# Kernel tuning notes

Measured on AMD Instinct MI355X. Metric: run time of the kernel, lower is better.

Reference implementation:

```python
import jax, jax.numpy as jnp
import numpy as np

N = 100_000   # nodes
E = 1_600_000 # edges
G = 128       # graphs in batch
DIN, DOUT = 100, 200


def setup_inputs() -> dict:
    key = jax.random.key(0)
    ks = jax.random.split(key, 12)
    def lin_w(k, fan_in, fan_out):
        return (jax.random.normal(k, (fan_in, fan_out), jnp.float32) / np.sqrt(fan_in)).astype(jnp.float32)
    return {
        "x": jax.random.normal(ks[0], (N, DIN), jnp.float32),
        "edge_index": jax.random.randint(ks[1], (2, E), 0, N, dtype=jnp.int32),
        "batch": jnp.sort(jax.random.randint(ks[2], (N,), 0, G, dtype=jnp.int32)),
        "W1": lin_w(ks[3], DIN, DOUT),  "b1": jnp.zeros((DOUT,), jnp.float32),
        "Wc": lin_w(ks[4], DOUT, DOUT), "bc": jnp.zeros((DOUT,), jnp.float32),
        "W2": lin_w(ks[5], DOUT, DOUT), "b2": jnp.zeros((DOUT,), jnp.float32),
        "W3": lin_w(ks[6], DOUT, DOUT), "b3": jnp.zeros((DOUT,), jnp.float32),
        "Wcls": lin_w(ks[7], DOUT, 2),  "bcls": jnp.zeros((2,), jnp.float32),
    }


def gcn_conv(x, W, b, src, dst, n_nodes):
    """PyG GCNConv: D^{-1/2}(A+I)D^{-1/2} X W + b, symmetric norm with self-loops."""
    h = x @ W  # [N, Dout]
    # degree at targets including the self-loop (+1)
    deg = jax.ops.segment_sum(jnp.ones((src.shape[0],), x.dtype), dst, num_segments=n_nodes) + 1.0
    dinv = jax.lax.rsqrt(deg)  # [N]
    # gather -> normalize -> scatter-add (messages along edges)
    msg = h[src] * (dinv[src] * dinv[dst])[:, None]          # [E, Dout]
    agg = jax.ops.segment_sum(msg, dst, num_segments=n_nodes)  # [N, Dout]
    # self-loop contribution handled analytically: norm_ii = dinv[i]^2
    agg = agg + h * (dinv * dinv)[:, None]
    return agg + b


def reference(x, edge_index, batch, W1, b1, Wc, bc, W2, b2, W3, b3, Wcls, bcls):
    src, dst = edge_index[0], edge_index[1]
    h = jax.nn.relu(gcn_conv(x, W1, b1, src, dst, N))
    # dropout is identity at eval time
    h = h @ Wc + bc
    h = jax.nn.relu(gcn_conv(h, W2, b2, src, dst, N))
    h = gcn_conv(h, W3, b3, src, dst, N)
    pooled = jax.ops.segment_max(h, batch, num_segments=G)  # global max pool -> [G, Dout]
    logits = pooled @ Wcls + bcls
    return jax.nn.softmax(logits, axis=1)
```

## Files before the change

### kernel.cpp

```cpp
#include <hip/hip_runtime.h>
#include <stdint.h>

#define N_NODES 100000
#define N_EDGES 1600000
#define N_GRAPHS 128
#define DIN 100
#define DOUT 200
#define LDH 200
#define LDX 128

#define NB 391
#define BCAP 5120
#define EPB 2048
#define NBLK 782

typedef unsigned short u16;
typedef unsigned int u32;
typedef _Float16 f16;
typedef f16 half8 __attribute__((ext_vector_type(8)));
typedef f16 half4 __attribute__((ext_vector_type(4)));
typedef f16 half2v __attribute__((ext_vector_type(2)));
typedef float floatx4 __attribute__((ext_vector_type(4)));

__device__ __forceinline__ float h2f(u16 h) {
  f16 x; __builtin_memcpy(&x, &h, 2); return (float)x;
}
__device__ __forceinline__ u16 f2h(float f) {
  f16 x = (f16)f; u16 r; __builtin_memcpy(&r, &x, 2); return r;
}
__device__ __forceinline__ u32 encmax(float f) {
  u32 b; __builtin_memcpy(&b, &f, 4);
  return (b & 0x80000000u) ? ~b : (b | 0x80000000u);
}

__device__ __forceinline__ void pack_frag(const float* __restrict__ W, int K, int nfrag,
                                          u16* __restrict__ out, int idx) {
  if (idx >= nfrag) return;
  int lane = idx & 63;
  int t = idx >> 6;
  int ct = t % 13, ks = t / 13;
  int n = ct * 16 + (lane & 15);
  int kbase = ks * 32 + (lane >> 4) * 8;
  u16 v[8];
  #pragma unroll
  for (int j = 0; j < 8; ++j) {
    int k = kbase + j;
    float f = (k < K && n < DOUT) ? W[(size_t)k * DOUT + n] : 0.f;
    v[j] = f2h(f);
  }
  uint4 o;
  o.x = (u32)v[0] | ((u32)v[1] << 16);
  o.y = (u32)v[2] | ((u32)v[3] << 16);
  o.z = (u32)v[4] | ((u32)v[5] << 16);
  o.w = (u32)v[6] | ((u32)v[7] << 16);
  *(uint4*)(out + (size_t)idx * 8) = o;
}

#define B_COMB  158
#define B_PK1   171
#define B_PK3   194
#define B_TOT   (194 + NBLK)
__global__ void k_prep(const int* __restrict__ dst, int* __restrict__ histAll,
                       const float* __restrict__ Wc, const float* __restrict__ bc,
                       const float* __restrict__ W2, float* __restrict__ Wc2,
                       float* __restrict__ bc2, const float* __restrict__ W1,
                       const float* __restrict__ W3, u16* __restrict__ Wpk1,
                       u16* __restrict__ Wpk3) {
  int b = blockIdx.x, t = threadIdx.x;
  if (b < B_COMB) {
    int gid = b * 256 + t;
    if (gid >= 201 * DOUT) return;
    int r = gid / DOUT, c = gid % DOUT;
    const float* a = (r < DOUT) ? (Wc + (size_t)r * DOUT) : bc;
    float s = 0.f;
    for (int k = 0; k < DOUT; ++k) s += a[k] * W2[(size_t)k * DOUT + c];
    if (r < DOUT) Wc2[(size_t)r * DOUT + c] = s;
    else bc2[c] = s;
  } else if (b < B_PK1) {
    pack_frag(W1, DIN, 4 * 13 * 64, Wpk1, (b - B_COMB) * 256 + t);
  } else if (b < B_PK3) {
    pack_frag(W3, DOUT, 7 * 13 * 64, Wpk3, (b - B_PK1) * 256 + t);
  } else {
    __shared__ int hist[NB];
    int hb = b - B_PK3;
    int e0 = hb * EPB;
    int e1 = min(e0 + EPB, N_EDGES);
    for (int j = t; j < NB; j += 256) hist[j] = 0;
    __syncthreads();
    for (int i = e0 + t; i < e1; i += 256)
      atomicAdd(&hist[dst[i] >> 8], 1);
    __syncthreads();
    for (int j = t; j < NB; j += 256)
      histAll[(size_t)hb * NB + j] = hist[j];
  }
}

#define SCAN_TOT (NB + 23)
__global__ void k_scan(const int* __restrict__ histAll, int* __restrict__ baseAll,
                       int* __restrict__ gcur, const float* __restrict__ Wc2,
                       u16* __restrict__ Wpk2) {
  int j = blockIdx.x, t = threadIdx.x;
  if (j >= NB) {
    pack_frag(Wc2, DOUT, 7 * 13 * 64, Wpk2, (j - NB) * 256 + t);
    return;
  }
  __shared__ int s[256];
  int run = 0;
  for (int c = 0; c < NBLK; c += 256) {
    int idx = c + t;
    int v = (idx < NBLK) ? histAll[(size_t)idx * NB + j] : 0;
    s[t] = v;
    __syncthreads();
    for (int o = 1; o < 256; o <<= 1) {
      int x = (t >= o) ? s[t - o] : 0;
      __syncthreads();
      s[t] += x;
      __syncthreads();
    }
    if (idx < NBLK) baseAll[(size_t)idx * NB + j] = run + s[t] - v;
    run += s[255];
    __syncthreads();
  }
  if (t == 0) gcur[j] = run;
}

__global__ void k_scatter(const int* __restrict__ src, const int* __restrict__ dst,
                          const int* __restrict__ baseAll, uint2* __restrict__ ebuf) {
  __shared__ int cur[NB];
  int b = blockIdx.x, t = threadIdx.x;
  int e0 = b * EPB;
  int e1 = min(e0 + EPB, N_EDGES);
  for (int j = t; j < NB; j += 256) cur[j] = baseAll[(size_t)b * NB + j];
  __syncthreads();
  for (int i = e0 + t; i < e1; i += 256) {
    int d = dst[i];
    int bk = d >> 8;
    int pos = atomicAdd(&cur[bk], 1);
    if (pos < BCAP)
      ebuf[(size_t)bk * BCAP + pos] = make_uint2((u32)d, (u32)src[i]);
  }
}

__global__ void k_csr(const uint2* __restrict__ ebuf, const int* __restrict__ gcur,
                      int* __restrict__ rowptr, float* __restrict__ dinv,
                      int* __restrict__ colv, const float* __restrict__ x,
                      u16* __restrict__ xs, u32* __restrict__ partenc) {
  __shared__ int s_cnt[256];
  __shared__ int s_cur[256];
  __shared__ int s_scan[256];
  __shared__ int s_g[NB];
  __shared__ int s_red[256];
  __shared__ float s_dinv[256];
  int b = blockIdx.x, t = threadIdx.x;
  int zid = b * 256 + t;
  if (zid < N_GRAPHS * DOUT) partenc[zid] = 0u;
  for (int j = t; j < NB; j += 256) s_g[j] = gcur[j];
  s_cnt[t] = 0;
  __syncthreads();
  int pacc = 0;
  for (int i = t; i < b; i += 256) pacc += s_g[i];
  s_red[t] = pacc;
  __syncthreads();
  for (int o = 128; o > 0; o >>= 1) {
    if (t < o) s_red[t] += s_red[t + o];
    __syncthreads();
  }
  int base = s_red[0];
  if (b == NB - 1 && t == 0) rowptr[N_NODES] = base + s_g[b];
  int cnt = s_g[b];
  int node0 = b << 8;
  const uint2* eb = ebuf + (size_t)b * BCAP;
  for (int i = t; i < cnt; i += 256)
    atomicAdd(&s_cnt[eb[i].x & 255], 1);
  __syncthreads();
  int v = s_cnt[t];
  s_scan[t] = v;
  __syncthreads();
  for (int o = 1; o < 256; o <<= 1) {
    int x2 = (t >= o) ? s_scan[t - o] : 0;
    __syncthreads();
    s_scan[t] += x2;
    __syncthreads();
  }
  int run = s_scan[t] - v;
  s_cur[t] = base + run;
  float dval = rsqrtf((float)v + 1.0f);
  s_dinv[t] = dval;
  int node = node0 + t;
  if (node < N_NODES) {
    rowptr[node] = base + run;
    dinv[node] = dval;
  }
  __syncthreads();
  for (int i = t; i < cnt; i += 256) {
    uint2 e = eb[i];
    int pos = atomicAdd(&s_cur[e.x & 255], 1);
    colv[pos] = (int)e.y;
  }
  for (int idx = t; idx < 256 * 50; idx += 256) {
    int nl = idx / 50, c = idx % 50;
    int nd = node0 + nl;
    if (nd < N_NODES) {
      float d = s_dinv[nl];
      float2 vv = *(const float2*)(x + (size_t)nd * DIN + c * 2);
      half2v o; o[0] = (f16)(d * vv.x); o[1] = (f16)(d * vv.y);
      *(half2v*)(xs + (size_t)nd * LDX + c * 2) = o;
    }
  }
}

template <int NKS>
__global__ __launch_bounds__(256) void k_gemm_mfma(const u16* __restrict__ A, int lda,
                                                   const u16* __restrict__ Wpk,
                                                   const float* __restrict__ bias,
                                                   const float* __restrict__ rowscale,
                                                   u16* __restrict__ C, int relu, int nrows) {
  int wv = threadIdx.x >> 6;
  int lane = threadIdx.x & 63;
  int r0 = blockIdx.x * 128 + wv * 32;
  int m = lane & 15, q = lane >> 4;
  int row0 = r0 + m, row1 = r0 + 16 + m;
  bool ok0 = (row0 < nrows), ok1 = (row1 < nrows);
  const u16* a0p = A + (size_t)row0 * lda + q * 8;
  const u16* a1p = A + (size_t)row1 * lda + q * 8;

  floatx4 acc0[13], acc1[13];
  #pragma unroll
  for (int ct = 0; ct < 13; ++ct) {
    acc0[ct] = floatx4{0.f, 0.f, 0.f, 0.f};
    acc1[ct] = floatx4{0.f, 0.f, 0.f, 0.f};
  }

  const u16* wp = Wpk + (size_t)lane * 8;
  #pragma unroll
  for (int ks = 0; ks < NKS; ++ks) {
    half8 a0 = ok0 ? *(const half8*)(a0p + ks * 32) : half8{0, 0, 0, 0, 0, 0, 0, 0};
    half8 a1 = ok1 ? *(const half8*)(a1p + ks * 32) : half8{0, 0, 0, 0, 0, 0, 0, 0};
    #pragma unroll
    for (int ct = 0; ct < 13; ++ct) {
      half8 bfr = *(const half8*)(wp + (size_t)(ks * 13 + ct) * 512);
      acc0[ct] = __builtin_amdgcn_mfma_f32_16x16x32_f16(a0, bfr, acc0[ct], 0, 0, 0);
      acc1[ct] = __builtin_amdgcn_mfma_f32_16x16x32_f16(a1, bfr, acc1[ct], 0, 0, 0);
    }
  }

  float sc0[4], sc1[4];
  #pragma unroll
  for (int rg = 0; rg < 4; ++rg) {
    int or0 = r0 + q * 4 + rg;
    int or1 = r0 + 16 + q * 4 + rg;
    sc0[rg] = (rowscale && or0 < nrows) ? rowscale[or0] : 1.f;
    sc1[rg] = (rowscale && or1 < nrows) ? rowscale[or1] : 1.f;
  }

  #pragma unroll
  for (int ct = 0; ct < 13; ++ct) {
    int c = ct * 16 + m;
    if (c >= DOUT) continue;
    float bv = bias ? bias[c] : 0.f;
    #pragma unroll
    for (int rg = 0; rg < 4; ++rg) {
      int or0 = r0 + q * 4 + rg;
      if (or0 < nrows) {
        float v = acc0[ct][rg] + bv;
        if (relu) v = fmaxf(v, 0.f);
        C[(size_t)or0 * LDH + c] = f2h(v * sc0[rg]);
      }
      int or1 = r0 + 16 + q * 4 + rg;
      if (or1 < nrows) {
        float v = acc1[ct][rg] + bv;
        if (relu) v = fmaxf(v, 0.f);
        C[(size_t)or1 * LDH + c] = f2h(v * sc1[rg]);
      }
    }
  }
}

__global__ void k_agg200h(const u16* __restrict__ T, const float* __restrict__ dinv,
                          const int* __restrict__ rowptr, const int* __restrict__ col,
                          const float* __restrict__ bias, u16* __restrict__ OUT,
                          int relu) {
  int wave = (blockIdx.x * blockDim.x + threadIdx.x) >> 6;
  int lane = threadIdx.x & 63;
  if (wave >= N_NODES || lane >= 50) return;
  int node = wave;
  int c4 = lane * 4;
  int beg = __builtin_amdgcn_readfirstlane(rowptr[node]);
  int end = __builtin_amdgcn_readfirstlane(rowptr[node + 1]);
  half4 sv = *(const half4*)(T + (size_t)node * LDH + c4);
  float di = dinv[node];
  float ax = 0.f, ay = 0.f, az = 0.f, aw = 0.f;
  int e = beg;
  for (; e + 16 <= end; e += 16) {
    int s[16];
    half4 tv[16];
    #pragma unroll
    for (int j = 0; j < 16; ++j) s[j] = col[e + j];
    #pragma unroll
    for (int j = 0; j < 16; ++j)
      tv[j] = *(const half4*)(T + (size_t)s[j] * LDH + c4);
    #pragma unroll
    for (int j = 0; j < 16; ++j) {
      ax += (float)tv[j][0]; ay += (float)tv[j][1];
      az += (float)tv[j][2]; aw += (float)tv[j][3];
    }
  }
  if (e + 8 <= end) {
    int s[8];
    half4 tv[8];
    #pragma unroll
    for (int j = 0; j < 8; ++j) s[j] = col[e + j];
    #pragma unroll
    for (int j = 0; j < 8; ++j)
      tv[j] = *(const half4*)(T + (size_t)s[j] * LDH + c4);
    #pragma unroll
    for (int j = 0; j < 8; ++j) {
      ax += (float)tv[j][0]; ay += (float)tv[j][1];
      az += (float)tv[j][2]; aw += (float)tv[j][3];
    }
    e += 8;
  }
  if (e + 4 <= end) {
    int s[4];
    half4 tv[4];
    #pragma unroll
    for (int j = 0; j < 4; ++j) s[j] = col[e + j];
    #pragma unroll
    for (int j = 0; j < 4; ++j)
      tv[j] = *(const half4*)(T + (size_t)s[j] * LDH + c4);
    #pragma unroll
    for (int j = 0; j < 4; ++j) {
      ax += (float)tv[j][0]; ay += (float)tv[j][1];
      az += (float)tv[j][2]; aw += (float)tv[j][3];
    }
    e += 4;
  }
  for (; e < end; ++e) {
    half4 tv = *(const half4*)(T + (size_t)col[e] * LDH + c4);
    ax += (float)tv[0]; ay += (float)tv[1];
    az += (float)tv[2]; aw += (float)tv[3];
  }
  float rx = di * (ax + (float)sv[0]);
  float ry = di * (ay + (float)sv[1]);
  float rz = di * (az + (float)sv[2]);
  float rw = di * (aw + (float)sv[3]);
  if (bias) {
    rx += bias[c4 + 0]; ry += bias[c4 + 1];
    rz += bias[c4 + 2]; rw += bias[c4 + 3];
  }
  if (relu) {
    rx = fmaxf(rx, 0.f); ry = fmaxf(ry, 0.f);
    rz = fmaxf(rz, 0.f); rw = fmaxf(rw, 0.f);
  }
  half4 o;
  o[0] = (f16)rx; o[1] = (f16)ry; o[2] = (f16)rz; o[3] = (f16)rw;
  __builtin_nontemporal_store(o, (half4*)(OUT + (size_t)node * LDH + c4));
}

__global__ void k_agg100h(const u16* __restrict__ T, const float* __restrict__ dinv,
                          const int* __restrict__ rowptr, const int* __restrict__ col,
                          u16* __restrict__ OUT) {
  int wave = (blockIdx.x * blockDim.x + threadIdx.x) >> 6;
  int lane = threadIdx.x & 63;
  if (wave >= N_NODES || lane >= 50) return;
  int node = wave;
  int c2 = lane * 2;
  int beg = __builtin_amdgcn_readfirstlane(rowptr[node]);
  int end = __builtin_amdgcn_readfirstlane(rowptr[node + 1]);
  half2v sv = *(const half2v*)(T + (size_t)node * LDX + c2);
  float di = dinv[node];
  float ax = 0.f, ay = 0.f;
  int e = beg;
  for (; e + 16 <= end; e += 16) {
    int s[16];
    half2v tv[16];
    #pragma unroll
    for (int j = 0; j < 16; ++j) s[j] = col[e + j];
    #pragma unroll
    for (int j = 0; j < 16; ++j)
      tv[j] = *(const half2v*)(T + (size_t)s[j] * LDX + c2);
    #pragma unroll
    for (int j = 0; j < 16; ++j) { ax += (float)tv[j][0]; ay += (float)tv[j][1]; }
  }
  if (e + 8 <= end) {
    int s[8];
    half2v tv[8];
    #pragma unroll
    for (int j = 0; j < 8; ++j) s[j] = col[e + j];
    #pragma unroll
    for (int j = 0; j < 8; ++j)
      tv[j] = *(const half2v*)(T + (size_t)s[j] * LDX + c2);
    #pragma unroll
    for (int j = 0; j < 8; ++j) { ax += (float)tv[j][0]; ay += (float)tv[j][1]; }
    e += 8;
  }
  if (e + 4 <= end) {
    int s[4];
    half2v tv[4];
    #pragma unroll
    for (int j = 0; j < 4; ++j) s[j] = col[e + j];
    #pragma unroll
    for (int j = 0; j < 4; ++j)
      tv[j] = *(const half2v*)(T + (size_t)s[j] * LDX + c2);
    #pragma unroll
    for (int j = 0; j < 4; ++j) { ax += (float)tv[j][0]; ay += (float)tv[j][1]; }
    e += 4;
  }
  for (; e < end; ++e) {
    half2v tv = *(const half2v*)(T + (size_t)col[e] * LDX + c2);
    ax += (float)tv[0]; ay += (float)tv[1];
  }
  half2v o;
  o[0] = (f16)(di * (ax + (float)sv[0]));
  o[1] = (f16)(di * (ay + (float)sv[1]));
  __builtin_nontemporal_store(o, (half2v*)(OUT + (size_t)node * LDX + c2));
}

__global__ void k_aggpool(const u16* __restrict__ T, const float* __restrict__ dinv,
                          const int* __restrict__ rowptr, const int* __restrict__ col,
                          const float* __restrict__ bias, const int* __restrict__ batch,
                          u32* __restrict__ partenc) {
  __shared__ u32 s_enc[4][DOUT];
  int t = threadIdx.x;
  for (int i = t; i < 4 * DOUT; i += 256) ((u32*)s_enc)[i] = 0u;
  __syncthreads();
  int wv = t >> 6, lane = t & 63;
  int nb0 = blockIdx.x * 16;
  int n0 = nb0 + wv * 4;
  int gfirst = batch[nb0];
  int rpl = rowptr[n0 + (lane < 4 ? lane : 4)];
  if (lane < 50) {
    int c4 = lane * 4;
    float b0 = bias[c4 + 0], b1v = bias[c4 + 1], b2v = bias[c4 + 2], b3v = bias[c4 + 3];
    for (int i = 0; i < 4; ++i) {
      int node = n0 + i;
      int beg = __builtin_amdgcn_readlane(rpl, i);
      int end = __builtin_amdgcn_readlane(rpl, i + 1);
      half4 sv = *(const half4*)(T + (size_t)node * LDH + c4);
      float di = dinv[node];
      float ax = 0.f, ay = 0.f, az = 0.f, aw = 0.f;
      int e = beg;
      for (; e + 16 <= end; e += 16) {
        int s[16];
        half4 tv[16];
        #pragma unroll
        for (int j = 0; j < 16; ++j) s[j] = col[e + j];
        #pragma unroll
        for (int j = 0; j < 16; ++j)
          tv[j] = *(const half4*)(T + (size_t)s[j] * LDH + c4);
        #pragma unroll
        for (int j = 0; j < 16; ++j) {
          ax += (float)tv[j][0]; ay += (float)tv[j][1];
          az += (float)tv[j][2]; aw += (float)tv[j][3];
        }
      }
      if (e + 8 <= end) {
        int s[8];
        half4 tv[8];
        #pragma unroll
        for (int j = 0; j < 8; ++j) s[j] = col[e + j];
        #pragma unroll
        for (int j = 0; j < 8; ++j)
          tv[j] = *(const half4*)(T + (size_t)s[j] * LDH + c4);
        #pragma unroll
        for (int j = 0; j < 8; ++j) {
          ax += (float)tv[j][0]; ay += (float)tv[j][1];
          az += (float)tv[j][2]; aw += (float)tv[j][3];
        }
        e += 8;
      }
      if (e + 4 <= end) {
        int s[4];
        half4 tv[4];
        #pragma unroll
        for (int j = 0; j < 4; ++j) s[j] = col[e + j];
        #pragma unroll
        for (int j = 0; j < 4; ++j)
          tv[j] = *(const half4*)(T + (size_t)s[j] * LDH + c4);
        #pragma unroll
        for (int j = 0; j < 4; ++j) {
          ax += (float)tv[j][0]; ay += (float)tv[j][1];
          az += (float)tv[j][2]; aw += (float)tv[j][3];
        }
        e += 4;
      }
      for (; e < end; ++e) {
        half4 tv = *(const half4*)(T + (size_t)col[e] * LDH + c4);
        ax += (float)tv[0]; ay += (float)tv[1];
        az += (float)tv[2]; aw += (float)tv[3];
      }
      float rx = di * (ax + (float)sv[0]) + b0;
      float ry = di * (ay + (float)sv[1]) + b1v;
      float rz = di * (az + (float)sv[2]) + b2v;
      float rw = di * (aw + (float)sv[3]) + b3v;
      u32 e0 = encmax(rx), e1 = encmax(ry), e2 = encmax(rz), e3 = encmax(rw);
      int slot = batch[node] - gfirst;
      if (slot < 4) {
        atomicMax(&s_enc[slot][c4 + 0], e0);
        atomicMax(&s_enc[slot][c4 + 1], e1);
        atomicMax(&s_enc[slot][c4 + 2], e2);
        atomicMax(&s_enc[slot][c4 + 3], e3);
      } else {
        u32* p = partenc + (size_t)batch[node] * DOUT + c4;
        atomicMax(&p[0], e0); atomicMax(&p[1], e1);
        atomicMax(&p[2], e2); atomicMax(&p[3], e3);
      }
    }
  }
  __syncthreads();
  for (int i = t; i < 4 * DOUT; i += 256) {
    u32 v = ((u32*)s_enc)[i];
    if (v) {
      int slot = i / DOUT, d = i % DOUT;
      atomicMax(&partenc[(size_t)(gfirst + slot) * DOUT + d], v);
    }
  }
}

__global__ void k_poolcls(const u32* __restrict__ partenc, const float* __restrict__ Wcls,
                          const float* __restrict__ bcls, float* __restrict__ out) {
  __shared__ float l0s[256], l1s[256];
  int g = blockIdx.x, t = threadIdx.x;
  float c0 = 0.f, c1 = 0.f;
  if (t < DOUT) {
    u32 e = partenc[(size_t)g * DOUT + t];
    float mv;
    if (e == 0u) {
      mv = -3.4e38f;
    } else {
      u32 b = (e & 0x80000000u) ? (e ^ 0x80000000u) : ~e;
      __builtin_memcpy(&mv, &b, 4);
    }
    c0 = mv * Wcls[t * 2 + 0];
    c1 = mv * Wcls[t * 2 + 1];
  }
  l0s[t] = c0; l1s[t] = c1;
  __syncthreads();
  for (int o = 128; o > 0; o >>= 1) {
    if (t < o) { l0s[t] += l0s[t + o]; l1s[t] += l1s[t + o]; }
    __syncthreads();
  }
  if (t == 0) {
    float l0 = l0s[0] + bcls[0], l1 = l1s[0] + bcls[1];
    float m = fmaxf(l0, l1);
    float e0 = expf(l0 - m), e1 = expf(l1 - m);
    float inv = 1.0f / (e0 + e1);
    out[g * 2 + 0] = e0 * inv;
    out[g * 2 + 1] = e1 * inv;
  }
}

static inline size_t align256(size_t x) { return (x + 255) & ~(size_t)255; }

extern "C" void kernel_launch(void* const* d_in, const int* in_sizes, int n_in,
                              void* d_out, int out_size, void* d_ws, size_t ws_size,
                              hipStream_t stream) {
  const float* x     = (const float*)d_in[0];
  const int*   ei    = (const int*)d_in[1];
  const int*   batch = (const int*)d_in[2];
  const float* W1    = (const float*)d_in[3];
  const float* b1    = (const float*)d_in[4];
  const float* Wc    = (const float*)d_in[5];
  const float* bc    = (const float*)d_in[6];
  const float* W2    = (const float*)d_in[7];
  const float* b2    = (const float*)d_in[8];
  const float* W3    = (const float*)d_in[9];
  const float* b3    = (const float*)d_in[10];
  const float* Wcls  = (const float*)d_in[11];
  const float* bcls  = (const float*)d_in[12];
  float* out = (float*)d_out;

  const int N = N_NODES, E = N_EDGES;
  const int* src = ei;
  const int* dst = ei + E;

  char* ws = (char*)d_ws;
  size_t off = 0;
  float* dinv    = (float*)(ws + off); off = align256(off + (size_t)N * 4);
  int*   rowptr  = (int*)  (ws + off); off = align256(off + (size_t)(N + 1) * 4);
  int*   col     = (int*)  (ws + off); off = align256(off + (size_t)E * 4);
  int*   gcur    = (int*)  (ws + off); off = align256(off + (size_t)NB * 4);
  int*   histAll = (int*)  (ws + off); off = align256(off + (size_t)NBLK * NB * 4);
  int*   baseAll = (int*)  (ws + off); off = align256(off + (size_t)NBLK * NB * 4);
  float* Wc2     = (float*)(ws + off); off = align256(off + (size_t)DOUT * DOUT * 4);
  float* bc2     = (float*)(ws + off); off = align256(off + (size_t)DOUT * 4);
  u16*   Wpk1    = (u16*)  (ws + off); off = align256(off + (size_t)4 * 13 * 64 * 8 * 2);
  u16*   Wpk2    = (u16*)  (ws + off); off = align256(off + (size_t)7 * 13 * 64 * 8 * 2);
  u16*   Wpk3    = (u16*)  (ws + off); off = align256(off + (size_t)7 * 13 * 64 * 8 * 2);
  u16*   xs      = (u16*)  (ws + off); off = align256(off + ((size_t)N * LDX + 128) * 2);
  u16*   bufX    = (u16*)  (ws + off); off = align256(off + ((size_t)N * LDX + 128) * 2);
  u16*   buf0    = (u16*)  (ws + off); off = align256(off + ((size_t)N * LDH + 128) * 2);
  u16*   buf1    = (u16*)  (ws + off); off = align256(off + ((size_t)N * LDH + 128) * 2);
  u16*   buf2    = (u16*)  (ws + off); off = align256(off + ((size_t)N * LDH + 128) * 2);

  uint2* ebuf    = (uint2*)buf0;
  u32*   partenc = (u32*)histAll;

  k_prep<<<B_TOT, 256, 0, stream>>>(dst, histAll, Wc, bc, W2, Wc2, bc2,
                                    W1, W3, Wpk1, Wpk3);
  k_scan<<<SCAN_TOT, 256, 0, stream>>>(histAll, baseAll, gcur, Wc2, Wpk2);
  k_scatter<<<NBLK, 256, 0, stream>>>(src, dst, baseAll, ebuf);
  k_csr<<<NB, 256, 0, stream>>>(ebuf, gcur, rowptr, dinv, col, x, xs, partenc);

  int gemmb = (N + 127) / 128;
  int aggb  = (N + 3) / 4;
  int aggpb = N / 16;

  k_agg100h<<<aggb, 256, 0, stream>>>(xs, dinv, rowptr, col, bufX);
  k_gemm_mfma<4><<<gemmb, 256, 0, stream>>>(bufX, LDX, Wpk1, b1, nullptr, buf0, 1, N);
  k_gemm_mfma<7><<<gemmb, 256, 0, stream>>>(buf0, LDH, Wpk2, bc2, dinv, buf2, 0, N);
  k_agg200h<<<aggb, 256, 0, stream>>>(buf2, dinv, rowptr, col, b2, buf0, 1);
  k_gemm_mfma<7><<<gemmb, 256, 0, stream>>>(buf0, LDH, Wpk3, nullptr, dinv, buf1, 0, N);
  k_aggpool<<<aggpb, 256, 0, stream>>>(buf1, dinv, rowptr, col, b3, batch, partenc);
  k_poolcls<<<N_GRAPHS, 256, 0, stream>>>(partenc, Wcls, bcls, out);
}
```

Before: 647.3 us.

## Fuse first-layer aggregation into MFMA GEMM and pack edge buffer to u32

The first GCN layer's neighbor aggregation and its GEMM are fused into one kernel. Each wave aggregates 32 rows into an LDS tile and then runs the MFMA product from it, so the intermediate aggregated buffer is no longer written to and read back from global memory. The scatter stage now packs source index and local destination into a single u32 instead of a uint2, halving edge-bucket traffic. The pooling kernel keeps a running max per graph segment and issues atomics only when the segment changes. The fused kernel has far fewer waves in flight during the latency-bound gather, since each wave handles 32 nodes in sequence, which may reduce latency hiding.

Measured after the change: 672.2 us. +3.9%, slower.

```diff
diff --git a/kernel.cpp b/kernel.cpp
--- a/kernel.cpp
+++ b/kernel.cpp
@@ -8,6 +8,7 @@
 #define DOUT 200
 #define LDH 200
 #define LDX 128
+#define LDT 136
 
 #define NB 391
 #define BCAP 5120
@@ -125,7 +126,7 @@
 }
 
 __global__ void k_scatter(const int* __restrict__ src, const int* __restrict__ dst,
-                          const int* __restrict__ baseAll, uint2* __restrict__ ebuf) {
+                          const int* __restrict__ baseAll, u32* __restrict__ ebuf) {
   __shared__ int cur[NB];
   int b = blockIdx.x, t = threadIdx.x;
   int e0 = b * EPB;
@@ -137,11 +138,11 @@
     int bk = d >> 8;
     int pos = atomicAdd(&cur[bk], 1);
     if (pos < BCAP)
-      ebuf[(size_t)bk * BCAP + pos] = make_uint2((u32)d, (u32)src[i]);
-  }
-}
-
-__global__ void k_csr(const uint2* __restrict__ ebuf, const int* __restrict__ gcur,
+      ebuf[(size_t)bk * BCAP + pos] = ((u32)src[i] << 8) | (u32)(d & 255);
+  }
+}
+
+__global__ void k_csr(const u32* __restrict__ ebuf, const int* __restrict__ gcur,
                       int* __restrict__ rowptr, float* __restrict__ dinv,
                       int* __restrict__ colv, const float* __restrict__ x,
                       u16* __restrict__ xs, u32* __restrict__ partenc) {
@@ -169,9 +170,9 @@
   if (b == NB - 1 && t == 0) rowptr[N_NODES] = base + s_g[b];
   int cnt = s_g[b];
   int node0 = b << 8;
-  const uint2* eb = ebuf + (size_t)b * BCAP;
+  const u32* eb = ebuf + (size_t)b * BCAP;
   for (int i = t; i < cnt; i += 256)
-    atomicAdd(&s_cnt[eb[i].x & 255], 1);
+    atomicAdd(&s_cnt[eb[i] & 255], 1);
   __syncthreads();
   int v = s_cnt[t];
   s_scan[t] = v;
@@ -193,9 +194,9 @@
   }
   __syncthreads();
   for (int i = t; i < cnt; i += 256) {
-    uint2 e = eb[i];
-    int pos = atomicAdd(&s_cur[e.x & 255], 1);
-    colv[pos] = (int)e.y;
+    u32 e = eb[i];
+    int pos = atomicAdd(&s_cur[e & 255], 1);
+    colv[pos] = (int)(e >> 8);
   }
   for (int idx = t; idx < 256 * 50; idx += 256) {
     int nl = idx / 50, c = idx % 50;
@@ -205,6 +206,123 @@
       float2 vv = *(const float2*)(x + (size_t)nd * DIN + c * 2);
       half2v o; o[0] = (f16)(d * vv.x); o[1] = (f16)(d * vv.y);
       *(half2v*)(xs + (size_t)nd * LDX + c * 2) = o;
+    }
+  }
+}
+
+__global__ __launch_bounds__(256) void k_aggemm1(const u16* __restrict__ T,
+                                                 const float* __restrict__ dinv,
+                                                 const int* __restrict__ rowptr,
+                                                 const int* __restrict__ col,
+                                                 const u16* __restrict__ Wpk1,
+                                                 const float* __restrict__ b1,
+                                                 u16* __restrict__ C, int nrows) {
+  __shared__ u16 tile[4][32][LDT];
+  int wv = threadIdx.x >> 6;
+  int lane = threadIdx.x & 63;
+  int r0 = blockIdx.x * 128 + wv * 32;
+  int rpl = rowptr[min(r0 + min(lane, 32), N_NODES)];
+  int dvb = ((const int*)dinv)[min(r0 + min(lane, 31), N_NODES - 1)];
+  int c2 = lane * 2;
+
+  for (int i = 0; i < 32; ++i) {
+    int node = r0 + i;
+    if (lane >= 50) {
+      *(half2v*)&tile[wv][i][100 + (lane - 50) * 2] = half2v{0, 0};
+      continue;
+    }
+    if (node >= nrows) {
+      *(half2v*)&tile[wv][i][c2] = half2v{0, 0};
+      continue;
+    }
+    int beg = __builtin_amdgcn_readlane(rpl, i);
+    int end = __builtin_amdgcn_readlane(rpl, i + 1);
+    int dib = __builtin_amdgcn_readlane(dvb, i);
+    float di; __builtin_memcpy(&di, &dib, 4);
+    half2v sv = *(const half2v*)(T + (size_t)node * LDX + c2);
+    float ax = 0.f, ay = 0.f;
+    int e = beg;
+    for (; e + 16 <= end; e += 16) {
+      int s[16];
+      half2v tv[16];
+      #pragma unroll
+      for (int j = 0; j < 16; ++j) s[j] = col[e + j];
+      #pragma unroll
+      for (int j = 0; j < 16; ++j)
+        tv[j] = *(const half2v*)(T + (size_t)s[j] * LDX + c2);
+      #pragma unroll
+      for (int j = 0; j < 16; ++j) { ax += (float)tv[j][0]; ay += (float)tv[j][1]; }
+    }
+    if (e + 8 <= end) {
+      int s[8];
+      half2v tv[8];
+      #pragma unroll
+      for (int j = 0; j < 8; ++j) s[j] = col[e + j];
+      #pragma unroll
+      for (int j = 0; j < 8; ++j)
+        tv[j] = *(const half2v*)(T + (size_t)s[j] * LDX + c2);
+      #pragma unroll
+      for (int j = 0; j < 8; ++j) { ax += (float)tv[j][0]; ay += (float)tv[j][1]; }
+      e += 8;
+    }
+    if (e + 4 <= end) {
+      int s[4];
+      half2v tv[4];
+      #pragma unroll
+      for (int j = 0; j < 4; ++j) s[j] = col[e + j];
+      #pragma unroll
+      for (int j = 0; j < 4; ++j)
+        tv[j] = *(const half2v*)(T + (size_t)s[j] * LDX + c2);
+      #pragma unroll
+      for (int j = 0; j < 4; ++j) { ax += (float)tv[j][0]; ay += (float)tv[j][1]; }
+      e += 4;
+    }
+    for (; e < end; ++e) {
+      half2v tv = *(const half2v*)(T + (size_t)col[e] * LDX + c2);
+      ax += (float)tv[0]; ay += (float)tv[1];
+    }
+    half2v o;
+    o[0] = (f16)(di * (ax + (float)sv[0]));
+    o[1] = (f16)(di * (ay + (float)sv[1]));
+    *(half2v*)&tile[wv][i][c2] = o;
+  }
+  __syncthreads();
+
+  int m = lane & 15, q = lane >> 4;
+  const u16* wp = Wpk1 + (size_t)lane * 8;
+  #pragma unroll
+  for (int half = 0; half < 2; ++half) {
+    int ct0 = half * 7;
+    int nct = half ? 6 : 7;
+    floatx4 acc0[7], acc1[7];
+    #pragma unroll
+    for (int c = 0; c < 7; ++c) {
+      acc0[c] = floatx4{0.f, 0.f, 0.f, 0.f};
+      acc1[c] = floatx4{0.f, 0.f, 0.f, 0.f};
+    }
+    #pragma unroll
+    for (int ks = 0; ks < 4; ++ks) {
+      half8 a0 = *(const half8*)&tile[wv][m][q * 8 + ks * 32];
+      half8 a1 = *(const half8*)&tile[wv][16 + m][q * 8 + ks * 32];
+      for (int c = 0; c < nct; ++c) {
+        half8 bfr = *(const half8*)(wp + (size_t)(ks * 13 + ct0 + c) * 512);
+        acc0[c] = __builtin_amdgcn_mfma_f32_16x16x32_f16(a0, bfr, acc0[c], 0, 0, 0);
+        acc1[c] = __builtin_amdgcn_mfma_f32_16x16x32_f16(a1, bfr, acc1[c], 0, 0, 0);
+      }
+    }
+    for (int c = 0; c < nct; ++c) {
+      int cc = (ct0 + c) * 16 + m;
+      if (cc >= DOUT) continue;
+      float bv = b1[cc];
+      #pragma unroll
+      for (int rg = 0; rg < 4; ++rg) {
+        int or0 = r0 + q * 4 + rg;
+        if (or0 < nrows)
+          C[(size_t)or0 * LDH + cc] = f2h(fmaxf(acc0[c][rg] + bv, 0.f));
+        int or1 = r0 + 16 + q * 4 + rg;
+        if (or1 < nrows)
+          C[(size_t)or1 * LDH + cc] = f2h(fmaxf(acc1[c][rg] + bv, 0.f));
+      }
     }
   }
 }
@@ -357,65 +475,6 @@
   __builtin_nontemporal_store(o, (half4*)(OUT + (size_t)node * LDH + c4));
 }
 
-__global__ void k_agg100h(const u16* __restrict__ T, const float* __restrict__ dinv,
-                          const int* __restrict__ rowptr, const int* __restrict__ col,
-                          u16* __restrict__ OUT) {
-  int wave = (blockIdx.x * blockDim.x + threadIdx.x) >> 6;
-  int lane = threadIdx.x & 63;
-  if (wave >= N_NODES || lane >= 50) return;
-  int node = wave;
-  int c2 = lane * 2;
-  int beg = __builtin_amdgcn_readfirstlane(rowptr[node]);
-  int end = __builtin_amdgcn_readfirstlane(rowptr[node + 1]);
-  half2v sv = *(const half2v*)(T + (size_t)node * LDX + c2);
-  float di = dinv[node];
-  float ax = 0.f, ay = 0.f;
-  int e = beg;
-  for (; e + 16 <= end; e += 16) {
-    int s[16];
-    half2v tv[16];
-    #pragma unroll
-    for (int j = 0; j < 16; ++j) s[j] = col[e + j];
-    #pragma unroll
-    for (int j = 0; j < 16; ++j)
-      tv[j] = *(const half2v*)(T + (size_t)s[j] * LDX + c2);
-    #pragma unroll
-    for (int j = 0; j < 16; ++j) { ax += (float)tv[j][0]; ay += (float)tv[j][1]; }
-  }
-  if (e + 8 <= end) {
-    int s[8];
-    half2v tv[8];
-    #pragma unroll
-    for (int j = 0; j < 8; ++j) s[j] = col[e + j];
-    #pragma unroll
-    for (int j = 0; j < 8; ++j)
-      tv[j] = *(const half2v*)(T + (size_t)s[j] * LDX + c2);
-    #pragma unroll
-    for (int j = 0; j < 8; ++j) { ax += (float)tv[j][0]; ay += (float)tv[j][1]; }
-    e += 8;
-  }
-  if (e + 4 <= end) {
-    int s[4];
-    half2v tv[4];
-    #pragma unroll
-    for (int j = 0; j < 4; ++j) s[j] = col[e + j];
-    #pragma unroll
-    for (int j = 0; j < 4; ++j)
-      tv[j] = *(const half2v*)(T + (size_t)s[j] * LDX + c2);
-    #pragma unroll
-    for (int j = 0; j < 4; ++j) { ax += (float)tv[j][0]; ay += (float)tv[j][1]; }
-    e += 4;
-  }
-  for (; e < end; ++e) {
-    half2v tv = *(const half2v*)(T + (size_t)col[e] * LDX + c2);
-    ax += (float)tv[0]; ay += (float)tv[1];
-  }
-  half2v o;
-  o[0] = (f16)(di * (ax + (float)sv[0]));
-  o[1] = (f16)(di * (ay + (float)sv[1]));
-  __builtin_nontemporal_store(o, (half2v*)(OUT + (size_t)node * LDX + c2));
-}
-
 __global__ void k_aggpool(const u16* __restrict__ T, const float* __restrict__ dinv,
                           const int* __restrict__ rowptr, const int* __restrict__ col,
                           const float* __restrict__ bias, const int* __restrict__ batch,
@@ -432,6 +491,8 @@
   if (lane < 50) {
     int c4 = lane * 4;
     float b0 = bias[c4 + 0], b1v = bias[c4 + 1], b2v = bias[c4 + 2], b3v = bias[c4 + 3];
+    float mx = 0.f, my = 0.f, mz = 0.f, mw = 0.f;
+    int curslot = -1;
     for (int i = 0; i < 4; ++i) {
       int node = n0 + i;
       int beg = __builtin_amdgcn_readlane(rpl, i);
@@ -493,17 +554,37 @@
       float ry = di * (ay + (float)sv[1]) + b1v;
       float rz = di * (az + (float)sv[2]) + b2v;
       float rw = di * (aw + (float)sv[3]) + b3v;
-      u32 e0 = encmax(rx), e1 = encmax(ry), e2 = encmax(rz), e3 = encmax(rw);
       int slot = batch[node] - gfirst;
-      if (slot < 4) {
-        atomicMax(&s_enc[slot][c4 + 0], e0);
-        atomicMax(&s_enc[slot][c4 + 1], e1);
-        atomicMax(&s_enc[slot][c4 + 2], e2);
-        atomicMax(&s_enc[slot][c4 + 3], e3);
+      if (slot != curslot) {
+        if (curslot >= 0) {
+          if (curslot < 4) {
+            atomicMax(&s_enc[curslot][c4 + 0], encmax(mx));
+            atomicMax(&s_enc[curslot][c4 + 1], encmax(my));
+            atomicMax(&s_enc[curslot][c4 + 2], encmax(mz));
+            atomicMax(&s_enc[curslot][c4 + 3], encmax(mw));
+          } else {
+            u32* p = partenc + (size_t)(gfirst + curslot) * DOUT + c4;
+            atomicMax(&p[0], encmax(mx)); atomicMax(&p[1], encmax(my));
+            atomicMax(&p[2], encmax(mz)); atomicMax(&p[3], encmax(mw));
+          }
+        }
+        curslot = slot;
+        mx = rx; my = ry; mz = rz; mw = rw;
       } else {
-        u32* p = partenc + (size_t)batch[node] * DOUT + c4;
-        atomicMax(&p[0], e0); atomicMax(&p[1], e1);
-        atomicMax(&p[2], e2); atomicMax(&p[3], e3);
+        mx = fmaxf(mx, rx); my = fmaxf(my, ry);
+        mz = fmaxf(mz, rz); mw = fmaxf(mw, rw);
+      }
+    }
+    if (curslot >= 0) {
+      if (curslot < 4) {
+        atomicMax(&s_enc[curslot][c4 + 0], encmax(mx));
+        atomicMax(&s_enc[curslot][c4 + 1], encmax(my));
+        atomicMax(&s_enc[curslot][c4 + 2], encmax(mz));
+        atomicMax(&s_enc[curslot][c4 + 3], encmax(mw));
+      } else {
+        u32* p = partenc + (size_t)(gfirst + curslot) * DOUT + c4;
+        atomicMax(&p[0], encmax(mx)); atomicMax(&p[1], encmax(my));
+        atomicMax(&p[2], encmax(mz)); atomicMax(&p[3], encmax(mw));
       }
     }
   }
@@ -588,12 +669,11 @@
   u16*   Wpk2    = (u16*)  (ws + off); off = align256(off + (size_t)7 * 13 * 64 * 8 * 2);
   u16*   Wpk3    = (u16*)  (ws + off); off = align256(off + (size_t)7 * 13 * 64 * 8 * 2);
   u16*   xs      = (u16*)  (ws + off); off = align256(off + ((size_t)N * LDX + 128) * 2);
-  u16*   bufX    = (u16*)  (ws + off); off = align256(off + ((size_t)N * LDX + 128) * 2);
   u16*   buf0    = (u16*)  (ws + off); off = align256(off + ((size_t)N * LDH + 128) * 2);
   u16*   buf1    = (u16*)  (ws + off); off = align256(off + ((size_t)N * LDH + 128) * 2);
   u16*   buf2    = (u16*)  (ws + off); off = align256(off + ((size_t)N * LDH + 128) * 2);
 
-  uint2* ebuf    = (uint2*)buf0;
+  u32*   ebuf    = (u32*)buf0;
   u32*   partenc = (u32*)histAll;
 
   k_prep<<<B_TOT, 256, 0, stream>>>(dst, histAll, Wc, bc, W2, Wc2, bc2,
@@ -606,8 +686,7 @@
   int aggb  = (N + 3) / 4;
   int aggpb = N / 16;
 
-  k_agg100h<<<aggb, 256, 0, stream>>>(xs, dinv, rowptr, col, bufX);
-  k_gemm_mfma<4><<<gemmb, 256, 0, stream>>>(bufX, LDX, Wpk1, b1, nullptr, buf0, 1, N);
+  k_aggemm1<<<gemmb, 256, 0, stream>>>(xs, dinv, rowptr, col, Wpk1, b1, buf0, N);
   k_gemm_mfma<7><<<gemmb, 256, 0, stream>>>(buf0, LDH, Wpk2, bc2, dinv, buf2, 0, N);
   k_agg200h<<<aggb, 256, 0, stream>>>(buf2, dinv, rowptr, col, b2, buf0, 1);
   k_gemm_mfma<7><<<gemmb, 256, 0, stream>>>(buf0, LDH, Wpk3, nullptr, dinv, buf1, 0, N);
```
